# Performance work log

Hardware: AMD Instinct MI355X
Metric: run time of the kernel (lower is better)

Reference implementation:

```python
import jax, jax.numpy as jnp
import numpy as np

B, T, E, A, D, S, N, K = 256, 64, 1024, 32, 1024, 256, 1024, 5
MIN_STD = 0.1


def setup_inputs() -> dict:
    key = jax.random.key(0)
    ks = jax.random.split(key, 16)
    def w(k, shape, scale=0.02):
        return jax.random.normal(k, shape, jnp.float32) * scale
    return dict(
        seq_len=T,
        obs_embed=jax.random.normal(ks[0], (B, T, E), jnp.float32),
        action=jax.random.normal(ks[1], (B, T, A), jnp.float32),
        nonterms=jnp.ones((B, T, 1), jnp.float32),
        init_deter=jax.random.normal(ks[2], (B, D), jnp.float32),
        init_stoch=jax.random.normal(ks[3], (B, S), jnp.float32),
        noise_prior=jax.random.normal(ks[4], (T - 1, B, S), jnp.float32),
        noise_post=jax.random.normal(ks[5], (T - 1, B, S), jnp.float32),
        W_embed=w(ks[6], (S + A, D)), b_embed=jnp.zeros((D,), jnp.float32),
        W_ens=w(ks[7], (K, D, S)), b_ens=jnp.zeros((K, S), jnp.float32),
        W_ih=w(ks[8], (3 * D, D)), W_hh=w(ks[9], (3 * D, D)),
        b_ih=jnp.zeros((3 * D,), jnp.float32), b_hh=jnp.zeros((3 * D,), jnp.float32),
        Wp1=w(ks[10], (D, N)), bp1=jnp.zeros((N,), jnp.float32),
        Wp2=w(ks[11], (N, 2 * S)), bp2=jnp.zeros((2 * S,), jnp.float32),
        Wq1=w(ks[12], (D + E, N)), bq1=jnp.zeros((N,), jnp.float32),
        Wq2=w(ks[13], (N, 2 * S)), bq2=jnp.zeros((2 * S,), jnp.float32),
    )


def _rollout(obs_embed, action, nonterms, init_deter, init_stoch,
             noise_prior, noise_post, W_embed, b_embed, W_ens, b_ens,
             W_ih, W_hh, b_ih, b_hh, Wp1, bp1, Wp2, bp2, Wq1, bq1, Wq2, bq2):
    elu = jax.nn.elu

    def gru(x, h):  # torch.nn.GRUCell math
        gi = x @ W_ih.T + b_ih
        gh = h @ W_hh.T + b_hh
        ir, iz, ig = jnp.split(gi, 3, axis=-1)
        hr, hz, hg = jnp.split(gh, 3, axis=-1)
        r = jax.nn.sigmoid(ir + hr)
        z = jax.nn.sigmoid(iz + hz)
        n = jnp.tanh(ig + r * hg)
        return (1.0 - z) * n + z * h

    def step(carry, xs):
        deter, stoch = carry
        obs_t, act_t, nt, eps_p, eps_q = xs  # nt: [B,1]
        prev_action = act_t * nt
        sa = elu(jnp.concatenate([stoch * nt, prev_action], -1) @ W_embed + b_embed)
        preds = jnp.einsum('bd,kds->kbs', sa, W_ens) + b_ens[:, None, :]  # ensemble heads
        deter_new = gru(sa, deter * nt)
        pm, ps = jnp.split(elu(deter_new @ Wp1 + bp1) @ Wp2 + bp2, 2, -1)
        ps = jax.nn.softplus(ps) + MIN_STD
        prior_stoch = pm + ps * eps_p
        qm, qs = jnp.split(elu(jnp.concatenate([deter_new, obs_t], -1) @ Wq1 + bq1) @ Wq2 + bq2, 2, -1)
        qs = jax.nn.softplus(qs) + MIN_STD
        post_stoch = qm + qs * eps_q
        prior_cat = jnp.concatenate([pm, ps, prior_stoch, deter_new], -1)   # [B, 3S+D]
        post_cat = jnp.concatenate([qm, qs, post_stoch, deter_new], -1)     # [B, 3S+D]
        disag_flat = jnp.transpose(preds, (1, 0, 2)).reshape(preds.shape[1], -1)  # [B, K*S]
        out = jnp.concatenate([prior_cat, post_cat, disag_flat], -1)
        return (deter_new, post_stoch), out

    Tm1 = noise_prior.shape[0]
    xs = (jnp.swapaxes(obs_embed[:, :Tm1], 0, 1),
          jnp.swapaxes(action[:, :Tm1], 0, 1),
          jnp.swapaxes(nonterms[:, :Tm1], 0, 1),
          noise_prior, noise_post)
    _, outs = jax.lax.scan(step, (init_deter, init_stoch), xs)
    return jnp.swapaxes(outs, 0, 1)  # [B, T-1, 2*(3S+D)+K*S]


def reference(seq_len, obs_embed, action, nonterms, init_deter, init_stoch,
              noise_prior, noise_post, W_embed, b_embed, W_ens, b_ens,
              W_ih, W_hh, b_ih, b_hh, Wp1, bp1, Wp2, bp2, Wq1, bq1, Wq2, bq2):
    return _rollout(obs_embed, action, nonterms, init_deter, init_stoch,
                    noise_prior, noise_post, W_embed, b_embed, W_ens, b_ens,
                    W_ih, W_hh, b_ih, b_hh, Wp1, bp1, Wp2, bp2, Wq1, bq1, Wq2, bq2)
```

## Files before the change

kernel.cpp:

```cpp
#include <hip/hip_runtime.h>

typedef float f32x4 __attribute__((ext_vector_type(4)));
typedef __bf16 bf16x8 __attribute__((ext_vector_type(8)));
typedef unsigned short u16;

#define OUTC 4864
#define OUTT ((size_t)63 * OUTC)

__device__ __forceinline__ u16 f2bf(float f) {
    unsigned u = __float_as_uint(f);
    u += 0x7FFFu + ((u >> 16) & 1u);
    return (u16)(u >> 16);
}
__device__ __forceinline__ float bf2f(u16 h) { return __uint_as_float((unsigned)h << 16); }
__device__ __forceinline__ float fexp(float x) { return __expf(x); }
__device__ __forceinline__ float eluf(float x) { return x > 0.f ? x : fexp(x) - 1.f; }
__device__ __forceinline__ float splus(float x) { return x > 15.f ? x : __logf(1.f + fexp(x)); }
__device__ __forceinline__ float sigm(float x) { return 1.f / (1.f + fexp(-x)); }
__device__ __forceinline__ float tanhfast(float x) { return 2.f / (1.f + fexp(-2.f * x)) - 1.f; }
__device__ __forceinline__ int swz(int row, int cb) { return row * 128 + (cb ^ ((row & 7) << 4)); }

template <int NT, class FA, class FE>
__device__ __forceinline__ void gemmN(char* As, FA fa, const u16* __restrict__ Bt,
                                      int ldb, int n0, int nstr, int K, int m0, FE fe) {
    char* Bs = As + 8192;
    const int tid = threadIdx.x;
    const int lane = tid & 63;
    const int w = tid >> 6;
    const int wr = (w >> 1) * 32, wc = (w & 1) * 32;
    f32x4 acc[NT][4];
    f32x4 zf = {0.f, 0.f, 0.f, 0.f};
#pragma unroll
    for (int j = 0; j < NT; j++)
#pragma unroll
        for (int q = 0; q < 4; q++) acc[j][q] = zf;
    const int r0 = tid >> 3;
    const int ke = (tid & 7) * 8;
    const int cb = (tid & 7) * 16;
    uint4 av0 = fa(m0 + r0, ke);
    uint4 av1 = fa(m0 + r0 + 32, ke);
    uint4 bv[NT][2];
#pragma unroll
    for (int j = 0; j < NT; j++) {
        bv[j][0] = *(const uint4*)(Bt + (size_t)(n0 + j * nstr + r0) * ldb + ke);
        bv[j][1] = *(const uint4*)(Bt + (size_t)(n0 + j * nstr + r0 + 32) * ldb + ke);
    }
    for (int k0 = 0; k0 < K; k0 += 64) {
        __syncthreads();
        *(uint4*)(As + swz(r0, cb)) = av0;
        *(uint4*)(As + swz(r0 + 32, cb)) = av1;
#pragma unroll
        for (int j = 0; j < NT; j++) {
            char* B = Bs + j * 8192;
            *(uint4*)(B + swz(r0, cb)) = bv[j][0];
            *(uint4*)(B + swz(r0 + 32, cb)) = bv[j][1];
        }
        __syncthreads();
        if (k0 + 64 < K) {
            int k1 = k0 + 64 + ke;
            av0 = fa(m0 + r0, k1);
            av1 = fa(m0 + r0 + 32, k1);
#pragma unroll
            for (int j = 0; j < NT; j++) {
                bv[j][0] = *(const uint4*)(Bt + (size_t)(n0 + j * nstr + r0) * ldb + k1);
                bv[j][1] = *(const uint4*)(Bt + (size_t)(n0 + j * nstr + r0 + 32) * ldb + k1);
            }
        }
#pragma unroll
        for (int kk = 0; kk < 64; kk += 32) {
            const int fcb = kk * 2 + (lane >> 4) * 16;
            bf16x8 a0 = *(const bf16x8*)(As + swz(wr + (lane & 15), fcb));
            bf16x8 a1 = *(const bf16x8*)(As + swz(wr + 16 + (lane & 15), fcb));
#pragma unroll
            for (int j = 0; j < NT; j++) {
                char* B = Bs + j * 8192;
                bf16x8 b0 = *(const bf16x8*)(B + swz(wc + (lane & 15), fcb));
                bf16x8 b1 = *(const bf16x8*)(B + swz(wc + 16 + (lane & 15), fcb));
                acc[j][0] = __builtin_amdgcn_mfma_f32_16x16x32_bf16(a0, b0, acc[j][0], 0, 0, 0);
                acc[j][1] = __builtin_amdgcn_mfma_f32_16x16x32_bf16(a0, b1, acc[j][1], 0, 0, 0);
                acc[j][2] = __builtin_amdgcn_mfma_f32_16x16x32_bf16(a1, b0, acc[j][2], 0, 0, 0);
                acc[j][3] = __builtin_amdgcn_mfma_f32_16x16x32_bf16(a1, b1, acc[j][3], 0, 0, 0);
            }
        }
    }
    const int er = (lane >> 4) * 4, ec = lane & 15;
#pragma unroll
    for (int q = 0; q < 4; q++) {
        int rr = m0 + wr + (q >> 1) * 16 + er;
        int cc = n0 + wc + (q & 1) * 16 + ec;
#pragma unroll
        for (int r = 0; r < 4; r++) {
            float vals[NT];
#pragma unroll
            for (int j = 0; j < NT; j++) vals[j] = acc[j][q][r];
            fe(rr + r, cc, vals);
        }
    }
}

template <int NT, class FA, class FE>
__device__ __forceinline__ void gemmS(char* sm, FA fa, const u16* __restrict__ Bt,
                                      int ldb, int n0, int nstr, int K, int m0, FE fe) {
    const int tid = threadIdx.x;
    const int lane = tid & 63;
    const int w = tid >> 6;
    const int kg = w >> 2;
    const int wi = w & 3;
    const int wr = (wi >> 1) * 32, wc = (wi & 1) * 32;
    const int Kh = K >> 1;
    const int kbase = kg * Kh;
    char* As = sm + kg * (1 + NT) * 8192;
    char* Bs = As + 8192;
    f32x4 acc[NT][4];
    f32x4 zf = {0.f, 0.f, 0.f, 0.f};
#pragma unroll
    for (int j = 0; j < NT; j++)
#pragma unroll
        for (int q = 0; q < 4; q++) acc[j][q] = zf;
    const int t2 = tid & 255;
    const int r0 = t2 >> 3;
    const int ke = (t2 & 7) * 8;
    const int cb = (t2 & 7) * 16;
    uint4 av0 = fa(m0 + r0, kbase + ke);
    uint4 av1 = fa(m0 + r0 + 32, kbase + ke);
    uint4 bv[NT][2];
#pragma unroll
    for (int j = 0; j < NT; j++) {
        bv[j][0] = *(const uint4*)(Bt + (size_t)(n0 + j * nstr + r0) * ldb + kbase + ke);
        bv[j][1] = *(const uint4*)(Bt + (size_t)(n0 + j * nstr + r0 + 32) * ldb + kbase + ke);
    }
    for (int k0 = 0; k0 < Kh; k0 += 64) {
        __syncthreads();
        *(uint4*)(As + swz(r0, cb)) = av0;
        *(uint4*)(As + swz(r0 + 32, cb)) = av1;
#pragma unroll
        for (int j = 0; j < NT; j++) {
            char* B = Bs + j * 8192;
            *(uint4*)(B + swz(r0, cb)) = bv[j][0];
            *(uint4*)(B + swz(r0 + 32, cb)) = bv[j][1];
        }
        __syncthreads();
        if (k0 + 64 < Kh) {
            int k1 = kbase + k0 + 64 + ke;
            av0 = fa(m0 + r0, k1);
            av1 = fa(m0 + r0 + 32, k1);
#pragma unroll
            for (int j = 0; j < NT; j++) {
                bv[j][0] = *(const uint4*)(Bt + (size_t)(n0 + j * nstr + r0) * ldb + k1);
                bv[j][1] = *(const uint4*)(Bt + (size_t)(n0 + j * nstr + r0 + 32) * ldb + k1);
            }
        }
#pragma unroll
        for (int kk = 0; kk < 64; kk += 32) {
            const int fcb = kk * 2 + (lane >> 4) * 16;
            bf16x8 a0 = *(const bf16x8*)(As + swz(wr + (lane & 15), fcb));
            bf16x8 a1 = *(const bf16x8*)(As + swz(wr + 16 + (lane & 15), fcb));
#pragma unroll
            for (int j = 0; j < NT; j++) {
                char* B = Bs + j * 8192;
                bf16x8 b0 = *(const bf16x8*)(B + swz(wc + (lane & 15), fcb));
                bf16x8 b1 = *(const bf16x8*)(B + swz(wc + 16 + (lane & 15), fcb));
                acc[j][0] = __builtin_amdgcn_mfma_f32_16x16x32_bf16(a0, b0, acc[j][0], 0, 0, 0);
                acc[j][1] = __builtin_amdgcn_mfma_f32_16x16x32_bf16(a0, b1, acc[j][1], 0, 0, 0);
                acc[j][2] = __builtin_amdgcn_mfma_f32_16x16x32_bf16(a1, b0, acc[j][2], 0, 0, 0);
                acc[j][3] = __builtin_amdgcn_mfma_f32_16x16x32_bf16(a1, b1, acc[j][3], 0, 0, 0);
            }
        }
    }
    __syncthreads();
    float* red = (float*)sm;
    const int slot = (wi * 64 + lane) * 16;
    if (kg == 1) {
#pragma unroll
        for (int j = 0; j < NT; j++)
#pragma unroll
            for (int q = 0; q < 4; q++)
#pragma unroll
                for (int r = 0; r < 4; r++)
                    red[j * 4096 + slot + q * 4 + r] = acc[j][q][r];
    }
    __syncthreads();
    if (kg == 0) {
        const int er = (lane >> 4) * 4, ec = lane & 15;
#pragma unroll
        for (int q = 0; q < 4; q++) {
            int rr = m0 + wr + (q >> 1) * 16 + er;
            int cc = n0 + wc + (q & 1) * 16 + ec;
#pragma unroll
            for (int r = 0; r < 4; r++) {
                float vals[NT];
#pragma unroll
                for (int j = 0; j < NT; j++)
                    vals[j] = acc[j][q][r] + red[j * 4096 + slot + q * 4 + r];
                fe(rr + r, cc, vals);
            }
        }
    }
}

#define PREP_BLOCKS 2048
#define PGSTR (PREP_BLOCKS * 256)
__device__ __forceinline__ void tpose(const float* __restrict__ in, u16* __restrict__ out,
                                      int R, int C, int Rpad, int total, int gtid) {
    for (int i = gtid; i < total; i += PGSTR) {
        int r = i % Rpad;
        int bc = i / Rpad;
        int c = bc % C;
        int bb = bc / C;
        out[i] = (r < R) ? f2bf(in[((size_t)bb * R + r) * C + c]) : (u16)0;
    }
}
__device__ __forceinline__ void castb(const float* __restrict__ in, u16* __restrict__ out,
                                      int total, int gtid) {
    for (int i = gtid; i < total; i += PGSTR) out[i] = f2bf(in[i]);
}

__global__ void __launch_bounds__(256) k_prep(
    const float* W_embed, const float* W_ih, const float* W_hh, const float* W_ens,
    const float* Wp1, const float* Wp2, const float* Wq1, const float* Wq2,
    u16* Wembed_t, u16* Wih_b, u16* Whh_b, u16* Wens_t,
    u16* Wp1_t, u16* Wp2_t, u16* Wq1d_t, u16* Wq1o_t, u16* Wq2_t,
    const float* init_deter, const float* init_stoch, const float* action,
    const float* nonterms, float* deter, u16* h_nt, u16* x_embed) {
    int gtid = blockIdx.x * 256 + threadIdx.x;
    tpose(W_embed, Wembed_t, 288, 1024, 320, 1024 * 320, gtid);
    castb(W_ih, Wih_b, 3072 * 1024, gtid);
    castb(W_hh, Whh_b, 3072 * 1024, gtid);
    tpose(W_ens, Wens_t, 1024, 256, 1024, 5 * 256 * 1024, gtid);
    tpose(Wp1, Wp1_t, 1024, 1024, 1024, 1024 * 1024, gtid);
    tpose(Wp2, Wp2_t, 1024, 512, 1024, 512 * 1024, gtid);
    tpose(Wq1, Wq1d_t, 1024, 1024, 1024, 1024 * 1024, gtid);
    tpose(Wq1 + 1024 * 1024, Wq1o_t, 1024, 1024, 1024, 1024 * 1024, gtid);
    tpose(Wq2, Wq2_t, 1024, 512, 1024, 512 * 1024, gtid);
    for (int idx = gtid; idx < 262144; idx += PGSTR) {
        int b = idx >> 10, d = idx & 1023;
        float nt0 = nonterms[b * 64];
        float dv = init_deter[idx];
        deter[idx] = dv;
        h_nt[idx] = f2bf(dv * nt0);
        if (d < 256) {
            x_embed[b * 320 + d] = f2bf(init_stoch[b * 256 + d] * nt0);
        } else if (d < 320) {
            int c = d - 256;
            x_embed[b * 320 + d] = (c < 32) ? f2bf(action[(size_t)b * 2048 + c] * nt0) : (u16)0;
        }
    }
}

__global__ void __launch_bounds__(256) k_obsc(const float* __restrict__ obs,
                                              const u16* __restrict__ Wq1o_t,
                                              u16* __restrict__ OBSC) {
    __shared__ char sm[40960];
    int bid = blockIdx.x;
    int rb = bid >> 2, cg = bid & 3;
    int m0 = rb * 64, n0 = cg * 256;
    auto fa = [&](int r, int k) {
        int tt = r >> 8, bb = r & 255;
        const float* p = obs + ((size_t)bb * 64 + tt) * 1024 + k;
        float4 f0 = *(const float4*)p, f1 = *(const float4*)(p + 4);
        union { u16 h[8]; uint4 q; } x;
        x.h[0] = f2bf(f0.x); x.h[1] = f2bf(f0.y); x.h[2] = f2bf(f0.z); x.h[3] = f2bf(f0.w);
        x.h[4] = f2bf(f1.x); x.h[5] = f2bf(f1.y); x.h[6] = f2bf(f1.z); x.h[7] = f2bf(f1.w);
        return x.q;
    };
    auto fe = [&](int r, int n, const float* v) {
#pragma unroll
        for (int j = 0; j < 4; j++) OBSC[(size_t)r * 1024 + n + j * 64] = f2bf(v[j]);
    };
    gemmN<4>(sm, fa, Wq1o_t, 1024, n0, 64, 1024, m0, fe);
}

__global__ void __launch_bounds__(256) k_sa(const u16* __restrict__ xe,
                                            const u16* __restrict__ Wt,
                                            const float* __restrict__ bias,
                                            u16* __restrict__ sa) {
    __shared__ char sm[16384];
    int m0 = blockIdx.y * 64, n0 = blockIdx.x * 64;
    auto fa = [&](int r, int k) { return *(const uint4*)(xe + r * 320 + k); };
    auto fe = [&](int r, int n, const float* v) {
        sa[r * 1024 + n] = f2bf(eluf(v[0] + bias[n]));
    };
    gemmN<1>(sm, fa, Wt, 320, n0, 0, 320, m0, fe);
}

__global__ void __launch_bounds__(512) k_gigh(const u16* __restrict__ sa,
                                              const u16* __restrict__ h_nt,
                                              const u16* __restrict__ Wih_b,
                                              const u16* __restrict__ Whh_b,
                                              const float* __restrict__ b_ih,
                                              const float* __restrict__ b_hh,
                                              float* __restrict__ gi,
                                              float* __restrict__ gh) {
    __shared__ char sm[32768];
    int bid = blockIdx.x;
    bool isgh = bid >= 192;
    int j = isgh ? bid - 192 : bid;
    int m0 = (j / 48) * 64, n0 = (j % 48) * 64;
    const u16* A = isgh ? h_nt : sa;
    const u16* B = isgh ? Whh_b : Wih_b;
    const float* bi = isgh ? b_hh : b_ih;
    float* dst = isgh ? gh : gi;
    auto fa = [&](int r, int k) { return *(const uint4*)(A + r * 1024 + k); };
    auto fe = [&](int r, int n, const float* v) { dst[(size_t)r * 3072 + n] = v[0] + bi[n]; };
    gemmS<1>(sm, fa, B, 1024, n0, 0, 1024, m0, fe);
}

__global__ void __launch_bounds__(256) k_gru(const float* __restrict__ gi,
                                             const float* __restrict__ gh,
                                             float* __restrict__ deter,
                                             const float* __restrict__ nonterms, int t,
                                             u16* __restrict__ deter_b,
                                             u16* __restrict__ h_nt,
                                             float* __restrict__ out) {
    int idx = blockIdx.x * 256 + threadIdx.x;
    int b = idx >> 10, d = idx & 1023;
    float nt = nonterms[b * 64 + t];
    float h = deter[idx] * nt;
    size_t gb = (size_t)b * 3072;
    float r = sigm(gi[gb + d] + gh[gb + d]);
    float z = sigm(gi[gb + 1024 + d] + gh[gb + 1024 + d]);
    float n = tanhfast(gi[gb + 2048 + d] + r * gh[gb + 2048 + d]);
    float dn = (1.f - z) * n + z * h;
    deter[idx] = dn;
    deter_b[idx] = f2bf(dn);
    h_nt[idx] = f2bf(dn * nonterms[b * 64 + t + 1]);
    float* ob = out + (size_t)b * OUTT + (size_t)t * OUTC;
    ob[768 + d] = dn;
    ob[2560 + d] = dn;
}

__global__ void __launch_bounds__(512) k_hpqe(const u16* __restrict__ deter_b,
                                              const u16* __restrict__ sa,
                                              const u16* __restrict__ Wp1_t,
                                              const u16* __restrict__ Wq1d_t,
                                              const u16* __restrict__ Wens_t,
                                              const float* __restrict__ bp1,
                                              const float* __restrict__ bq1,
                                              const float* __restrict__ b_ens,
                                              const u16* __restrict__ OBSC,
                                              u16* __restrict__ HP,
                                              u16* __restrict__ HQ,
                                              float* __restrict__ out, int t) {
    __shared__ char sm[32768];
    int bid = blockIdx.x;
    if (bid < 128) {
        bool isq = bid >= 64;
        int j = bid & 63;
        int m0 = (j >> 4) * 64, n0 = (j & 15) * 64;
        const u16* B = isq ? Wq1d_t : Wp1_t;
        const float* bi = isq ? bq1 : bp1;
        u16* dst = isq ? HQ : HP;
        const u16* ob = OBSC + (size_t)t * 262144;
        auto fa = [&](int r, int k) { return *(const uint4*)(deter_b + r * 1024 + k); };
        auto fe = [&](int r, int n, const float* v) {
            float x = v[0] + bi[n];
            if (isq) x += bf2f(ob[r * 1024 + n]);
            dst[r * 1024 + n] = f2bf(eluf(x));
        };
        gemmS<1>(sm, fa, B, 1024, n0, 0, 1024, m0, fe);
    } else {
        int j = bid - 128;
        int m0 = (j / 20) * 64, n0 = (j % 20) * 64;
        float* op = out + (size_t)t * OUTC + 3584;
        auto fa = [&](int r, int k) { return *(const uint4*)(sa + r * 1024 + k); };
        auto fe = [&](int r, int n, const float* v) {
            op[(size_t)r * OUTT + n] = v[0] + b_ens[n];
        };
        gemmS<1>(sm, fa, Wens_t, 1024, n0, 0, 1024, m0, fe);
    }
}

__global__ void __launch_bounds__(512) k_pqdist(const u16* __restrict__ HP,
                                                const u16* __restrict__ HQ,
                                                const u16* __restrict__ Wp2_t,
                                                const u16* __restrict__ Wq2_t,
                                                const float* __restrict__ bp2,
                                                const float* __restrict__ bq2,
                                                const float* __restrict__ noise_p,
                                                const float* __restrict__ noise_q,
                                                const float* __restrict__ nonterms,
                                                const float* __restrict__ action,
                                                float* __restrict__ out,
                                                u16* __restrict__ x_embed, int t) {
    __shared__ char sm[49152];
    int bid = blockIdx.x;
    if (bid < 32) {
        bool isq = bid >= 16;
        int j = bid & 15;
        int m0 = (j >> 2) * 64, n0 = (j & 3) * 64;
        const u16* A = isq ? HQ : HP;
        const u16* B = isq ? Wq2_t : Wp2_t;
        const float* b2 = isq ? bq2 : bp2;
        const float* noise = isq ? noise_q : noise_p;
        int obase = isq ? 1792 : 0;
        auto fa = [&](int r, int k) { return *(const uint4*)(A + r * 1024 + k); };
        auto fe = [&](int r, int s, const float* v) {
            float m = v[0] + b2[s];
            float sd = splus(v[1] + b2[s + 256]) + 0.1f;
            float eps = noise[(size_t)t * 65536 + r * 256 + s];
            float st = m + sd * eps;
            float* obp = out + (size_t)r * OUTT + (size_t)t * OUTC + obase;
            obp[s] = m;
            obp[256 + s] = sd;
            obp[512 + s] = st;
            if (isq) {
                float ntn = nonterms[r * 64 + t + 1];
                x_embed[r * 320 + s] = f2bf(st * ntn);
            }
        };
        gemmS<2>(sm, fa, B, 1024, n0, 256, 1024, m0, fe);
    } else {
        for (int i = (bid - 32) * 512 + threadIdx.x; i < 8192; i += 2048) {
            int b = i >> 5, c = i & 31;
            float ntn = nonterms[b * 64 + t + 1];
            x_embed[b * 320 + 256 + c] =
                f2bf(action[(size_t)b * 2048 + (size_t)(t + 1) * 32 + c] * ntn);
        }
    }
}

extern "C" void kernel_launch(void* const* d_in, const int* in_sizes, int n_in,
                              void* d_out, int out_size, void* d_ws, size_t ws_size,
                              hipStream_t stream) {
    const float* obs = (const float*)d_in[1];
    const float* action = (const float*)d_in[2];
    const float* nonterms = (const float*)d_in[3];
    const float* init_deter = (const float*)d_in[4];
    const float* init_stoch = (const float*)d_in[5];
    const float* noise_p = (const float*)d_in[6];
    const float* noise_q = (const float*)d_in[7];
    const float* W_embed = (const float*)d_in[8];
    const float* b_embed = (const float*)d_in[9];
    const float* W_ens = (const float*)d_in[10];
    const float* b_ens = (const float*)d_in[11];
    const float* W_ih = (const float*)d_in[12];
    const float* W_hh = (const float*)d_in[13];
    const float* b_ih = (const float*)d_in[14];
    const float* b_hh = (const float*)d_in[15];
    const float* Wp1 = (const float*)d_in[16];
    const float* bp1 = (const float*)d_in[17];
    const float* Wp2 = (const float*)d_in[18];
    const float* bp2 = (const float*)d_in[19];
    const float* Wq1 = (const float*)d_in[20];
    const float* bq1 = (const float*)d_in[21];
    const float* Wq2 = (const float*)d_in[22];
    const float* bq2 = (const float*)d_in[23];
    float* out = (float*)d_out;

    char* ws = (char*)d_ws;
    size_t off = 0;
    auto alloc = [&](size_t bytes) {
        void* p = ws + off;
        off += (bytes + 255) & ~(size_t)255;
        return p;
    };
    u16* Wembed_t = (u16*)alloc((size_t)1024 * 320 * 2);
    u16* Wih_b = (u16*)alloc((size_t)3072 * 1024 * 2);
    u16* Whh_b = (u16*)alloc((size_t)3072 * 1024 * 2);
    u16* Wens_t = (u16*)alloc((size_t)1280 * 1024 * 2);
    u16* Wp1_t = (u16*)alloc((size_t)1024 * 1024 * 2);
    u16* Wp2_t = (u16*)alloc((size_t)512 * 1024 * 2);
    u16* Wq1d_t = (u16*)alloc((size_t)1024 * 1024 * 2);
    u16* Wq1o_t = (u16*)alloc((size_t)1024 * 1024 * 2);
    u16* Wq2_t = (u16*)alloc((size_t)512 * 1024 * 2);
    u16* OBSC = (u16*)alloc((size_t)16128 * 1024 * 2);
    u16* x_embed = (u16*)alloc((size_t)256 * 320 * 2);
    u16* h_nt = (u16*)alloc((size_t)256 * 1024 * 2);
    u16* sa = (u16*)alloc((size_t)256 * 1024 * 2);
    u16* deter_b = (u16*)alloc((size_t)256 * 1024 * 2);
    u16* HP = (u16*)alloc((size_t)256 * 1024 * 2);
    u16* HQ = (u16*)alloc((size_t)256 * 1024 * 2);
    float* deter = (float*)alloc((size_t)256 * 1024 * 4);
    float* gi = (float*)alloc((size_t)256 * 3072 * 4);
    float* gh = (float*)alloc((size_t)256 * 3072 * 4);
    (void)ws_size; (void)in_sizes; (void)n_in; (void)out_size;

    k_prep<<<PREP_BLOCKS, 256, 0, stream>>>(
        W_embed, W_ih, W_hh, W_ens, Wp1, Wp2, Wq1, Wq2,
        Wembed_t, Wih_b, Whh_b, Wens_t, Wp1_t, Wp2_t, Wq1d_t, Wq1o_t, Wq2_t,
        init_deter, init_stoch, action, nonterms, deter, h_nt, x_embed);
    k_obsc<<<1008, 256, 0, stream>>>(obs, Wq1o_t, OBSC);

    for (int t = 0; t < 63; t++) {
        k_sa<<<dim3(16, 4), 256, 0, stream>>>(x_embed, Wembed_t, b_embed, sa);
        k_gigh<<<384, 512, 0, stream>>>(sa, h_nt, Wih_b, Whh_b, b_ih, b_hh, gi, gh);
        k_gru<<<1024, 256, 0, stream>>>(gi, gh, deter, nonterms, t, deter_b, h_nt, out);
        k_hpqe<<<208, 512, 0, stream>>>(deter_b, sa, Wp1_t, Wq1d_t, Wens_t,
                                        bp1, bq1, b_ens, OBSC, HP, HQ, out, t);
        k_pqdist<<<36, 512, 0, stream>>>(HP, HQ, Wp2_t, Wq2_t, bp2, bq2,
                                         noise_p, noise_q, nonterms, action,
                                         out, x_embed, t);
    }
}
```

Before: 5.850 ms.

## Fuse GRU gate math into input GEMM, overlap embed and hidden GEMMs, drop split-K

```diff
diff --git a/kernel.cpp b/kernel.cpp
--- a/kernel.cpp
+++ b/kernel.cpp
@@ -94,106 +94,6 @@
 #pragma unroll
             for (int j = 0; j < NT; j++) vals[j] = acc[j][q][r];
             fe(rr + r, cc, vals);
-        }
-    }
-}
-
-template <int NT, class FA, class FE>
-__device__ __forceinline__ void gemmS(char* sm, FA fa, const u16* __restrict__ Bt,
-                                      int ldb, int n0, int nstr, int K, int m0, FE fe) {
-    const int tid = threadIdx.x;
-    const int lane = tid & 63;
-    const int w = tid >> 6;
-    const int kg = w >> 2;
-    const int wi = w & 3;
-    const int wr = (wi >> 1) * 32, wc = (wi & 1) * 32;
-    const int Kh = K >> 1;
-    const int kbase = kg * Kh;
-    char* As = sm + kg * (1 + NT) * 8192;
-    char* Bs = As + 8192;
-    f32x4 acc[NT][4];
-    f32x4 zf = {0.f, 0.f, 0.f, 0.f};
-#pragma unroll
-    for (int j = 0; j < NT; j++)
-#pragma unroll
-        for (int q = 0; q < 4; q++) acc[j][q] = zf;
-    const int t2 = tid & 255;
-    const int r0 = t2 >> 3;
-    const int ke = (t2 & 7) * 8;
-    const int cb = (t2 & 7) * 16;
-    uint4 av0 = fa(m0 + r0, kbase + ke);
-    uint4 av1 = fa(m0 + r0 + 32, kbase + ke);
-    uint4 bv[NT][2];
-#pragma unroll
-    for (int j = 0; j < NT; j++) {
-        bv[j][0] = *(const uint4*)(Bt + (size_t)(n0 + j * nstr + r0) * ldb + kbase + ke);
-        bv[j][1] = *(const uint4*)(Bt + (size_t)(n0 + j * nstr + r0 + 32) * ldb + kbase + ke);
-    }
-    for (int k0 = 0; k0 < Kh; k0 += 64) {
-        __syncthreads();
-        *(uint4*)(As + swz(r0, cb)) = av0;
-        *(uint4*)(As + swz(r0 + 32, cb)) = av1;
-#pragma unroll
-        for (int j = 0; j < NT; j++) {
-            char* B = Bs + j * 8192;
-            *(uint4*)(B + swz(r0, cb)) = bv[j][0];
-            *(uint4*)(B + swz(r0 + 32, cb)) = bv[j][1];
-        }
-        __syncthreads();
-        if (k0 + 64 < Kh) {
-            int k1 = kbase + k0 + 64 + ke;
-            av0 = fa(m0 + r0, k1);
-            av1 = fa(m0 + r0 + 32, k1);
-#pragma unroll
-            for (int j = 0; j < NT; j++) {
-                bv[j][0] = *(const uint4*)(Bt + (size_t)(n0 + j * nstr + r0) * ldb + k1);
-                bv[j][1] = *(const uint4*)(Bt + (size_t)(n0 + j * nstr + r0 + 32) * ldb + k1);
-            }
-        }
-#pragma unroll
-        for (int kk = 0; kk < 64; kk += 32) {
-            const int fcb = kk * 2 + (lane >> 4) * 16;
-            bf16x8 a0 = *(const bf16x8*)(As + swz(wr + (lane & 15), fcb));
-            bf16x8 a1 = *(const bf16x8*)(As + swz(wr + 16 + (lane & 15), fcb));
-#pragma unroll
-            for (int j = 0; j < NT; j++) {
-                char* B = Bs + j * 8192;
-                bf16x8 b0 = *(const bf16x8*)(B + swz(wc + (lane & 15), fcb));
-                bf16x8 b1 = *(const bf16x8*)(B + swz(wc + 16 + (lane & 15), fcb));
-                acc[j][0] = __builtin_amdgcn_mfma_f32_16x16x32_bf16(a0, b0, acc[j][0], 0, 0, 0);
-                acc[j][1] = __builtin_amdgcn_mfma_f32_16x16x32_bf16(a0, b1, acc[j][1], 0, 0, 0);
-                acc[j][2] = __builtin_amdgcn_mfma_f32_16x16x32_bf16(a1, b0, acc[j][2], 0, 0, 0);
-                acc[j][3] = __builtin_amdgcn_mfma_f32_16x16x32_bf16(a1, b1, acc[j][3], 0, 0, 0);
-            }
-        }
-    }
-    __syncthreads();
-    float* red = (float*)sm;
-    const int slot = (wi * 64 + lane) * 16;
-    if (kg == 1) {
-#pragma unroll
-        for (int j = 0; j < NT; j++)
-#pragma unroll
-            for (int q = 0; q < 4; q++)
-#pragma unroll
-                for (int r = 0; r < 4; r++)
-                    red[j * 4096 + slot + q * 4 + r] = acc[j][q][r];
-    }
-    __syncthreads();
-    if (kg == 0) {
-        const int er = (lane >> 4) * 4, ec = lane & 15;
-#pragma unroll
-        for (int q = 0; q < 4; q++) {
-            int rr = m0 + wr + (q >> 1) * 16 + er;
-            int cc = n0 + wc + (q & 1) * 16 + ec;
-#pragma unroll
-            for (int r = 0; r < 4; r++) {
-                float vals[NT];
-#pragma unroll
-                for (int j = 0; j < NT; j++)
-                    vals[j] = acc[j][q][r] + red[j * 4096 + slot + q * 4 + r];
-                fe(rr + r, cc, vals);
-            }
         }
     }
 }
@@ -270,66 +170,62 @@
     gemmN<4>(sm, fa, Wq1o_t, 1024, n0, 64, 1024, m0, fe);
 }
 
-__global__ void __launch_bounds__(256) k_sa(const u16* __restrict__ xe,
-                                            const u16* __restrict__ Wt,
-                                            const float* __restrict__ bias,
-                                            u16* __restrict__ sa) {
+__global__ void __launch_bounds__(256) k_sa_gh(const u16* __restrict__ xe,
+                                               const u16* __restrict__ Wembed_t,
+                                               const float* __restrict__ b_embed,
+                                               u16* __restrict__ sa,
+                                               const u16* __restrict__ h_nt,
+                                               const u16* __restrict__ Whh_b,
+                                               const float* __restrict__ b_hh,
+                                               float* __restrict__ gh) {
     __shared__ char sm[16384];
+    int bid = blockIdx.x;
+    if (bid < 64) {
+        int m0 = (bid >> 4) * 64, n0 = (bid & 15) * 64;
+        auto fa = [&](int r, int k) { return *(const uint4*)(xe + r * 320 + k); };
+        auto fe = [&](int r, int n, const float* v) {
+            sa[r * 1024 + n] = f2bf(eluf(v[0] + b_embed[n]));
+        };
+        gemmN<1>(sm, fa, Wembed_t, 320, n0, 0, 320, m0, fe);
+    } else {
+        int j = bid - 64;
+        int m0 = (j / 48) * 64, n0 = (j % 48) * 64;
+        auto fa = [&](int r, int k) { return *(const uint4*)(h_nt + r * 1024 + k); };
+        auto fe = [&](int r, int n, const float* v) { gh[(size_t)r * 3072 + n] = v[0] + b_hh[n]; };
+        gemmN<1>(sm, fa, Whh_b, 1024, n0, 0, 1024, m0, fe);
+    }
+}
+
+__global__ void __launch_bounds__(256) k_gi_gru(const u16* __restrict__ sa,
+                                                const u16* __restrict__ Wih_b,
+                                                const float* __restrict__ b_ih,
+                                                const float* __restrict__ gh,
+                                                const float* __restrict__ nonterms,
+                                                float* __restrict__ deter,
+                                                u16* __restrict__ deter_b,
+                                                u16* __restrict__ h_nt,
+                                                float* __restrict__ out, int t) {
+    __shared__ char sm[32768];
     int m0 = blockIdx.y * 64, n0 = blockIdx.x * 64;
-    auto fa = [&](int r, int k) { return *(const uint4*)(xe + r * 320 + k); };
-    auto fe = [&](int r, int n, const float* v) {
-        sa[r * 1024 + n] = f2bf(eluf(v[0] + bias[n]));
+    auto fa = [&](int r, int k) { return *(const uint4*)(sa + r * 1024 + k); };
+    auto fe = [&](int r, int d, const float* v) {
+        size_t gb = (size_t)r * 3072;
+        float rg = sigm(v[0] + b_ih[d] + gh[gb + d]);
+        float zg = sigm(v[1] + b_ih[1024 + d] + gh[gb + 1024 + d]);
+        float ng = tanhfast(v[2] + b_ih[2048 + d] + rg * gh[gb + 2048 + d]);
+        float h = deter[r * 1024 + d] * nonterms[r * 64 + t];
+        float dn = (1.f - zg) * ng + zg * h;
+        deter[r * 1024 + d] = dn;
+        deter_b[r * 1024 + d] = f2bf(dn);
+        h_nt[r * 1024 + d] = f2bf(dn * nonterms[r * 64 + t + 1]);
+        float* ob = out + (size_t)r * OUTT + (size_t)t * OUTC;
+        ob[768 + d] = dn;
+        ob[2560 + d] = dn;
     };
-    gemmN<1>(sm, fa, Wt, 320, n0, 0, 320, m0, fe);
-}
-
-__global__ void __launch_bounds__(512) k_gigh(const u16* __restrict__ sa,
-                                              const u16* __restrict__ h_nt,
-                                              const u16* __restrict__ Wih_b,
-                                              const u16* __restrict__ Whh_b,
-                                              const float* __restrict__ b_ih,
-                                              const float* __restrict__ b_hh,
-                                              float* __restrict__ gi,
-                                              float* __restrict__ gh) {
-    __shared__ char sm[32768];
-    int bid = blockIdx.x;
-    bool isgh = bid >= 192;
-    int j = isgh ? bid - 192 : bid;
-    int m0 = (j / 48) * 64, n0 = (j % 48) * 64;
-    const u16* A = isgh ? h_nt : sa;
-    const u16* B = isgh ? Whh_b : Wih_b;
-    const float* bi = isgh ? b_hh : b_ih;
-    float* dst = isgh ? gh : gi;
-    auto fa = [&](int r, int k) { return *(const uint4*)(A + r * 1024 + k); };
-    auto fe = [&](int r, int n, const float* v) { dst[(size_t)r * 3072 + n] = v[0] + bi[n]; };
-    gemmS<1>(sm, fa, B, 1024, n0, 0, 1024, m0, fe);
-}
-
-__global__ void __launch_bounds__(256) k_gru(const float* __restrict__ gi,
-                                             const float* __restrict__ gh,
-                                             float* __restrict__ deter,
-                                             const float* __restrict__ nonterms, int t,
-                                             u16* __restrict__ deter_b,
-                                             u16* __restrict__ h_nt,
-                                             float* __restrict__ out) {
-    int idx = blockIdx.x * 256 + threadIdx.x;
-    int b = idx >> 10, d = idx & 1023;
-    float nt = nonterms[b * 64 + t];
-    float h = deter[idx] * nt;
-    size_t gb = (size_t)b * 3072;
-    float r = sigm(gi[gb + d] + gh[gb + d]);
-    float z = sigm(gi[gb + 1024 + d] + gh[gb + 1024 + d]);
-    float n = tanhfast(gi[gb + 2048 + d] + r * gh[gb + 2048 + d]);
-    float dn = (1.f - z) * n + z * h;
-    deter[idx] = dn;
-    deter_b[idx] = f2bf(dn);
-    h_nt[idx] = f2bf(dn * nonterms[b * 64 + t + 1]);
-    float* ob = out + (size_t)b * OUTT + (size_t)t * OUTC;
-    ob[768 + d] = dn;
-    ob[2560 + d] = dn;
-}
-
-__global__ void __launch_bounds__(512) k_hpqe(const u16* __restrict__ deter_b,
+    gemmN<3>(sm, fa, Wih_b, 1024, n0, 1024, 1024, m0, fe);
+}
+
+__global__ void __launch_bounds__(256) k_hpqe(const u16* __restrict__ deter_b,
                                               const u16* __restrict__ sa,
                                               const u16* __restrict__ Wp1_t,
                                               const u16* __restrict__ Wq1d_t,
@@ -341,7 +237,7 @@
                                               u16* __restrict__ HP,
                                               u16* __restrict__ HQ,
                                               float* __restrict__ out, int t) {
-    __shared__ char sm[32768];
+    __shared__ char sm[16384];
     int bid = blockIdx.x;
     if (bid < 128) {
         bool isq = bid >= 64;
@@ -357,7 +253,7 @@
             if (isq) x += bf2f(ob[r * 1024 + n]);
             dst[r * 1024 + n] = f2bf(eluf(x));
         };
-        gemmS<1>(sm, fa, B, 1024, n0, 0, 1024, m0, fe);
+        gemmN<1>(sm, fa, B, 1024, n0, 0, 1024, m0, fe);
     } else {
         int j = bid - 128;
         int m0 = (j / 20) * 64, n0 = (j % 20) * 64;
@@ -366,11 +262,11 @@
         auto fe = [&](int r, int n, const float* v) {
             op[(size_t)r * OUTT + n] = v[0] + b_ens[n];
         };
-        gemmS<1>(sm, fa, Wens_t, 1024, n0, 0, 1024, m0, fe);
-    }
-}
-
-__global__ void __launch_bounds__(512) k_pqdist(const u16* __restrict__ HP,
+        gemmN<1>(sm, fa, Wens_t, 1024, n0, 0, 1024, m0, fe);
+    }
+}
+
+__global__ void __launch_bounds__(256) k_pqdist(const u16* __restrict__ HP,
                                                 const u16* __restrict__ HQ,
                                                 const u16* __restrict__ Wp2_t,
                                                 const u16* __restrict__ Wq2_t,
@@ -382,7 +278,7 @@
                                                 const float* __restrict__ action,
                                                 float* __restrict__ out,
                                                 u16* __restrict__ x_embed, int t) {
-    __shared__ char sm[49152];
+    __shared__ char sm[24576];
     int bid = blockIdx.x;
     if (bid < 32) {
         bool isq = bid >= 16;
@@ -408,9 +304,9 @@
                 x_embed[r * 320 + s] = f2bf(st * ntn);
             }
         };
-        gemmS<2>(sm, fa, B, 1024, n0, 256, 1024, m0, fe);
+        gemmN<2>(sm, fa, B, 1024, n0, 256, 1024, m0, fe);
     } else {
-        for (int i = (bid - 32) * 512 + threadIdx.x; i < 8192; i += 2048) {
+        for (int i = (bid - 32) * 256 + threadIdx.x; i < 8192; i += 1024) {
             int b = i >> 5, c = i & 31;
             float ntn = nonterms[b * 64 + t + 1];
             x_embed[b * 320 + 256 + c] =
@@ -471,7 +367,6 @@
     u16* HP = (u16*)alloc((size_t)256 * 1024 * 2);
     u16* HQ = (u16*)alloc((size_t)256 * 1024 * 2);
     float* deter = (float*)alloc((size_t)256 * 1024 * 4);
-    float* gi = (float*)alloc((size_t)256 * 3072 * 4);
     float* gh = (float*)alloc((size_t)256 * 3072 * 4);
     (void)ws_size; (void)in_sizes; (void)n_in; (void)out_size;
 
@@ -482,12 +377,13 @@
     k_obsc<<<1008, 256, 0, stream>>>(obs, Wq1o_t, OBSC);
 
     for (int t = 0; t < 63; t++) {
-        k_sa<<<dim3(16, 4), 256, 0, stream>>>(x_embed, Wembed_t, b_embed, sa);
-        k_gigh<<<384, 512, 0, stream>>>(sa, h_nt, Wih_b, Whh_b, b_ih, b_hh, gi, gh);
-        k_gru<<<1024, 256, 0, stream>>>(gi, gh, deter, nonterms, t, deter_b, h_nt, out);
-        k_hpqe<<<208, 512, 0, stream>>>(deter_b, sa, Wp1_t, Wq1d_t, Wens_t,
+        k_sa_gh<<<256, 256, 0, stream>>>(x_embed, Wembed_t, b_embed, sa,
+                                         h_nt, Whh_b, b_hh, gh);
+        k_gi_gru<<<dim3(16, 4), 256, 0, stream>>>(sa, Wih_b, b_ih, gh, nonterms,
+                                                  deter, deter_b, h_nt, out, t);
+        k_hpqe<<<208, 256, 0, stream>>>(deter_b, sa, Wp1_t, Wq1d_t, Wens_t,
                                         bp1, bq1, b_ens, OBSC, HP, HQ, out, t);
-        k_pqdist<<<36, 512, 0, stream>>>(HP, HQ, Wp2_t, Wq2_t, bp2, bq2,
+        k_pqdist<<<36, 256, 0, stream>>>(HP, HQ, Wp2_t, Wq2_t, bp2, bq2,
                                          noise_p, noise_q, nonterms, action,
                                          out, x_embed, t);
     }
```

Measured after the change: 7.962 ms. 1.36x slower.
